# Optimization experiments

Measured on AMD Instinct MI355X. Metric: run time of the kernel, lower is better.

The kernel has to match this reference:

```python
import jax, jax.numpy as jnp
import numpy as np

N_NODES = 50000
N_EDGES = 800000
F_IN = 64
F_OUT = 64
SELF_LOOP_W = 2.0  # GCNConv improved=True


def setup_inputs() -> dict:
    key = jax.random.key(0)
    k1, k2, k3 = jax.random.split(key, 3)
    x = jax.random.normal(k1, (N_NODES, F_IN), dtype=jnp.float32)
    edge_index = jax.random.randint(k2, (2, N_EDGES), 0, N_NODES, dtype=jnp.int64)
    W = jax.random.normal(k3, (F_IN, F_OUT), dtype=jnp.float32) / np.sqrt(F_IN)
    b = jnp.zeros((F_OUT,), dtype=jnp.float32)
    return {"x": x, "edge_index": edge_index, "W": W, "b": b}


def reference(x, edge_index, W, b):
    N = x.shape[0]
    E = edge_index.shape[1]
    src, dst = edge_index[0], edge_index[1]
    # add self loops with weight 2.0 (improved=True)
    loop = jnp.arange(N, dtype=src.dtype)
    src_f = jnp.concatenate([src, loop])
    dst_f = jnp.concatenate([dst, loop])
    w_edge = jnp.concatenate([jnp.ones((E,), x.dtype), jnp.full((N,), SELF_LOOP_W, x.dtype)])
    # symmetric normalization: deg over target nodes (PyG gcn_norm)
    deg = jax.ops.segment_sum(w_edge, dst_f, num_segments=N)
    dinv = jnp.where(deg > 0, deg ** -0.5, 0.0)
    norm = dinv[src_f] * w_edge * dinv[dst_f]  # [E+N]
    # dense transform, then gather-scale-scatter
    h = x @ W  # [N, F_OUT]
    agg = jax.ops.segment_sum(norm[:, None] * h[src_f], dst_f, num_segments=N)
    out = jax.nn.relu(agg + b)
    return jax.nn.log_softmax(out, axis=1)
```

## Files before the change

kernel.cpp:

```cpp
#include <hip/hip_runtime.h>
#include <hip/hip_fp16.h>

#define N_NODES 50000
#define N_EDGES 800000
#define F 64
#define NB ((N_NODES + 255) / 256)
#define NBUCK 98
#define BSHIFT 9
#define BCAP 12288
#define P1_BLOCKS ((N_EDGES + 1023) / 1024)
#define NPB 32


union H2U { __half2 h; unsigned u; };

__global__ void k_init(int* __restrict__ bcur) {
    int t = threadIdx.x;
    if (t < NBUCK) bcur[t] = t * BCAP;
}

__global__ __launch_bounds__(1024) void k_p1(const int* __restrict__ src,
                                             const int* __restrict__ dst,
                                             int* __restrict__ bcur,
                                             int* __restrict__ staging) {
    __shared__ int lcnt[NBUCK];
    __shared__ int lbase[NBUCK];
    int t = threadIdx.x;
    if (t < NBUCK) lcnt[t] = 0;
    __syncthreads();
    int e = blockIdx.x * 1024 + t;
    int s = 0, d = 0, bk = 0, rank = 0;
    bool valid = (e < N_EDGES);
    if (valid) {
        s = src[e]; d = dst[e];
        bk = d >> BSHIFT;
        rank = atomicAdd(&lcnt[bk], 1);
    }
    __syncthreads();
    if (t < NBUCK && lcnt[t]) lbase[t] = atomicAdd(&bcur[t], lcnt[t]);
    __syncthreads();
    if (valid)
        staging[lbase[bk] + rank] = ((d & 511) << 16) | s;
}

__global__ __launch_bounds__(1024) void k_p23(const int* __restrict__ staging,
                                              const int* __restrict__ bcur,
                                              int* __restrict__ offsets,
                                              int* __restrict__ counts,
                                              float* __restrict__ dinv,
                                              int* __restrict__ pack) {
    __shared__ int ncnt[512];
    __shared__ int lcur[512];
    int t = threadIdx.x;
    int b = blockIdx.x;
    int nb0 = b << BSHIFT;
    if (t < 512) ncnt[t] = 0;
    __syncthreads();
    int beg = b * BCAP, end = bcur[b];
    for (int i = beg + t; i < end; i += 1024)
        atomicAdd(&ncnt[staging[i] >> 16], 1);
    __syncthreads();
    int c = (t < 512) ? ncnt[t] : 0;
    for (int off = 1; off < 512; off <<= 1) {
        int u = (t < 512 && t >= off) ? ncnt[t - off] : 0;
        __syncthreads();
        if (t < 512) ncnt[t] += u;
        __syncthreads();
    }
    if (t < 512) {
        int goff = beg + (ncnt[t] - c);
        lcur[t] = goff;
        int node = nb0 + t;
        if (node < N_NODES) {
            offsets[node] = goff;
            counts[node]  = c;
            dinv[node]    = rsqrtf((float)c + 2.0f);
        }
    }
    __syncthreads();
    for (int i = beg + t; i < end; i += 1024) {
        int v = staging[i];
        int pos = atomicAdd(&lcur[v >> 16], 1);
        pack[pos] = v & 0xFFFF;
    }
}

__global__ __launch_bounds__(256) void k_convert(const float4* __restrict__ x4,
                                                 uint2* __restrict__ xh8) {
    int t = blockIdx.x * 256 + threadIdx.x;
    float4 v = x4[t];
    H2U a, b;
    a.h = __float22half2_rn(make_float2(v.x, v.y));
    b.h = __float22half2_rn(make_float2(v.z, v.w));
    uint2 o; o.x = a.u; o.y = b.u;
    xh8[t] = o;
}

__global__ __launch_bounds__(512) void k_agg(const float* __restrict__ x,
                                             const __half* __restrict__ xh,
                                             const float* __restrict__ dinv,
                                             const int* __restrict__ offsets,
                                             const int* __restrict__ counts,
                                             const int* __restrict__ pack,
                                             const float* __restrict__ W,
                                             const float* __restrict__ bias,
                                             float* __restrict__ out) {
    __shared__ unsigned sWu[F * F / 2];
    __shared__ float srow[NPB][F];
    int t = threadIdx.x;
    for (int i = t; i < F * F / 2; i += 512) {
        int p = i >> 6, c = i & 63;
        H2U u;
        u.h = __float22half2_rn(make_float2(W[(2 * p) * F + c], W[(2 * p + 1) * F + c]));
        sWu[i] = u.u;
    }
    __syncthreads();

    int wid = t >> 6, lane = t & 63;
    int qe = lane >> 4, qc = lane & 15;
    int nbase = blockIdx.x * NPB + wid * 4;
    const uint2* xh8 = reinterpret_cast<const uint2*>(xh);

    int  begs[4], degs[4], pls[4];
    float dns[4], nms[4];
#pragma unroll
    for (int i = 0; i < 4; ++i) {
        int n = nbase + i;
        if (n < N_NODES) {
            begs[i] = offsets[n]; degs[i] = counts[n]; dns[i] = dinv[n];
        } else { begs[i] = 0; degs[i] = 0; dns[i] = 0.f; }
    }
#pragma unroll
    for (int i = 0; i < 4; ++i) {
        int s = 0; float nm = 0.f;
        if (lane < degs[i]) {
            s = pack[begs[i] + lane];
            nm = dns[i] * dinv[s];
        }
        pls[i] = s; nms[i] = nm;
    }

#pragma unroll
    for (int i = 0; i < 4; i += 2) {
        float a00 = 0.f, a01 = 0.f, a02 = 0.f, a03 = 0.f;
        float a10 = 0.f, a11 = 0.f, a12 = 0.f, a13 = 0.f;
        int lim = min(max(degs[i], degs[i + 1]), 64);
        for (int r = 0; r < lim; r += 8) {
            int e0 = r + qe, e1 = r + 4 + qe;
            int   s00 = __shfl(pls[i], e0);     float m00 = __shfl(nms[i], e0);
            int   s01 = __shfl(pls[i], e1);     float m01 = __shfl(nms[i], e1);
            int   s10 = __shfl(pls[i + 1], e0); float m10 = __shfl(nms[i + 1], e0);
            int   s11 = __shfl(pls[i + 1], e1); float m11 = __shfl(nms[i + 1], e1);
            uint2 v00 = xh8[(size_t)s00 * 16 + qc];
            uint2 v01 = xh8[(size_t)s01 * 16 + qc];
            uint2 v10 = xh8[(size_t)s10 * 16 + qc];
            uint2 v11 = xh8[(size_t)s11 * 16 + qc];
            H2U u0, u1; float2 f;
            u0.u = v00.x; u1.u = v00.y;
            f = __half22float2(u0.h); a00 = fmaf(m00, f.x, a00); a01 = fmaf(m00, f.y, a01);
            f = __half22float2(u1.h); a02 = fmaf(m00, f.x, a02); a03 = fmaf(m00, f.y, a03);
            u0.u = v01.x; u1.u = v01.y;
            f = __half22float2(u0.h); a00 = fmaf(m01, f.x, a00); a01 = fmaf(m01, f.y, a01);
            f = __half22float2(u1.h); a02 = fmaf(m01, f.x, a02); a03 = fmaf(m01, f.y, a03);
            u0.u = v10.x; u1.u = v10.y;
            f = __half22float2(u0.h); a10 = fmaf(m10, f.x, a10); a11 = fmaf(m10, f.y, a11);
            f = __half22float2(u1.h); a12 = fmaf(m10, f.x, a12); a13 = fmaf(m10, f.y, a13);
            u0.u = v11.x; u1.u = v11.y;
            f = __half22float2(u0.h); a10 = fmaf(m11, f.x, a10); a11 = fmaf(m11, f.y, a11);
            f = __half22float2(u1.h); a12 = fmaf(m11, f.x, a12); a13 = fmaf(m11, f.y, a13);
        }
#pragma unroll
        for (int k = 0; k < 2; ++k) {
            int dend = begs[i + k] + degs[i + k];
            for (int base = begs[i + k] + 64; base < dend; base += 8) {
                int e0 = base + qe, e1 = base + 4 + qe;
                int s0 = 0, s1 = 0; float m0 = 0.f, m1 = 0.f;
                if (e0 < dend) { s0 = pack[e0]; m0 = dns[i + k] * dinv[s0]; }
                if (e1 < dend) { s1 = pack[e1]; m1 = dns[i + k] * dinv[s1]; }
                uint2 r0 = xh8[(size_t)s0 * 16 + qc];
                uint2 r1 = xh8[(size_t)s1 * 16 + qc];
                H2U u0, u1; float2 f;
                float* A = (k == 0) ? &a00 : &a10;
                u0.u = r0.x; u1.u = r0.y;
                f = __half22float2(u0.h); A[0] = fmaf(m0, f.x, A[0]); A[1] = fmaf(m0, f.y, A[1]);
                f = __half22float2(u1.h); A[2] = fmaf(m0, f.x, A[2]); A[3] = fmaf(m0, f.y, A[3]);
                u0.u = r1.x; u1.u = r1.y;
                f = __half22float2(u0.h); A[0] = fmaf(m1, f.x, A[0]); A[1] = fmaf(m1, f.y, A[1]);
                f = __half22float2(u1.h); A[2] = fmaf(m1, f.x, A[2]); A[3] = fmaf(m1, f.y, A[3]);
            }
        }
        a00 += __shfl_xor(a00, 16); a10 += __shfl_xor(a10, 16);
        a01 += __shfl_xor(a01, 16); a11 += __shfl_xor(a11, 16);
        a02 += __shfl_xor(a02, 16); a12 += __shfl_xor(a12, 16);
        a03 += __shfl_xor(a03, 16); a13 += __shfl_xor(a13, 16);
        a00 += __shfl_xor(a00, 32); a10 += __shfl_xor(a10, 32);
        a01 += __shfl_xor(a01, 32); a11 += __shfl_xor(a11, 32);
        a02 += __shfl_xor(a02, 32); a12 += __shfl_xor(a12, 32);
        a03 += __shfl_xor(a03, 32); a13 += __shfl_xor(a13, 32);
        if (qe == 0) {
            int n0 = nbase + i;
            if (n0 < N_NODES) {
                float c2 = 2.0f * dns[i] * dns[i];
                float4 xv = reinterpret_cast<const float4*>(x + (size_t)n0 * F)[qc];
                a00 = fmaf(c2, xv.x, a00); a01 = fmaf(c2, xv.y, a01);
                a02 = fmaf(c2, xv.z, a02); a03 = fmaf(c2, xv.w, a03);
                float4 w; w.x = a00; w.y = a01; w.z = a02; w.w = a03;
                *reinterpret_cast<float4*>(&srow[wid * 4 + i][qc * 4]) = w;
            }
            int n1 = nbase + i + 1;
            if (n1 < N_NODES) {
                float c2 = 2.0f * dns[i + 1] * dns[i + 1];
                float4 xv = reinterpret_cast<const float4*>(x + (size_t)n1 * F)[qc];
                a10 = fmaf(c2, xv.x, a10); a11 = fmaf(c2, xv.y, a11);
                a12 = fmaf(c2, xv.z, a12); a13 = fmaf(c2, xv.w, a13);
                float4 w; w.x = a10; w.y = a11; w.z = a12; w.w = a13;
                *reinterpret_cast<float4*>(&srow[wid * 4 + i + 1][qc * 4]) = w;
            }
        }
    }

    asm volatile("s_waitcnt lgkmcnt(0)" ::: "memory");

    float bl = bias[lane];
    float y0 = bl, y1 = bl, y2 = bl, y3 = bl;
#pragma unroll 4
    for (int j = 0; j < 16; ++j) {
        float4 r0 = *reinterpret_cast<const float4*>(&srow[wid * 4 + 0][j * 4]);
        float4 r1 = *reinterpret_cast<const float4*>(&srow[wid * 4 + 1][j * 4]);
        float4 r2 = *reinterpret_cast<const float4*>(&srow[wid * 4 + 2][j * 4]);
        float4 r3 = *reinterpret_cast<const float4*>(&srow[wid * 4 + 3][j * 4]);
        H2U ua, ub;
        ua.u = sWu[(2 * j) * F + lane];
        ub.u = sWu[(2 * j + 1) * F + lane];
        float2 wab = __half22float2(ua.h);
        float2 wcd = __half22float2(ub.h);
        y0 = fmaf(r0.x, wab.x, y0); y0 = fmaf(r0.y, wab.y, y0); y0 = fmaf(r0.z, wcd.x, y0); y0 = fmaf(r0.w, wcd.y, y0);
        y1 = fmaf(r1.x, wab.x, y1); y1 = fmaf(r1.y, wab.y, y1); y1 = fmaf(r1.z, wcd.x, y1); y1 = fmaf(r1.w, wcd.y, y1);
        y2 = fmaf(r2.x, wab.x, y2); y2 = fmaf(r2.y, wab.y, y2); y2 = fmaf(r2.z, wcd.x, y2); y2 = fmaf(r2.w, wcd.y, y2);
        y3 = fmaf(r3.x, wab.x, y3); y3 = fmaf(r3.y, wab.y, y3); y3 = fmaf(r3.z, wcd.x, y3); y3 = fmaf(r3.w, wcd.y, y3);
    }

    float ys[4] = { y0, y1, y2, y3 };
#pragma unroll
    for (int i = 0; i < 4; ++i) {
        float y = fmaxf(ys[i], 0.0f);
        float mx = y;
#pragma unroll
        for (int off = 32; off > 0; off >>= 1)
            mx = fmaxf(mx, __shfl_xor(mx, off));
        float ex = __expf(y - mx);
        float ss = ex;
#pragma unroll
        for (int off = 32; off > 0; off >>= 1)
            ss += __shfl_xor(ss, off);
        int n = nbase + i;
        if (n < N_NODES) out[n * F + lane] = y - mx - __logf(ss);
    }
}


__global__ void k_count_b(const int* __restrict__ dst, int* __restrict__ counts) {
    int e = blockIdx.x * blockDim.x + threadIdx.x;
    if (e < N_EDGES) atomicAdd(&counts[dst[e]], 1);
}
__global__ __launch_bounds__(256) void k_blocksum(const int* __restrict__ counts,
                                                  int* __restrict__ bs) {
    __shared__ int sh[256];
    int t = threadIdx.x;
    int g = blockIdx.x * 256 + t;
    int v = (g < N_NODES) ? counts[g] : 0;
    sh[t] = v;
    __syncthreads();
    for (int off = 128; off > 0; off >>= 1) {
        if (t < off) sh[t] += sh[t + off];
        __syncthreads();
    }
    if (t == 0) bs[blockIdx.x] = sh[0];
}
__global__ __launch_bounds__(256) void k_scanblocks(int* __restrict__ bs) {
    __shared__ int sh[256];
    int t = threadIdx.x;
    int v = (t < NB) ? bs[t] : 0;
    sh[t] = v;
    __syncthreads();
    for (int off = 1; off < 256; off <<= 1) {
        int u = (t >= off) ? sh[t - off] : 0;
        __syncthreads();
        sh[t] += u;
        __syncthreads();
    }
    if (t < NB) bs[t] = sh[t] - v;
}
__global__ __launch_bounds__(256) void k_offsets_b(int* __restrict__ counts,
                                                   const int* __restrict__ bs,
                                                   int* __restrict__ offsets,
                                                   float* __restrict__ dinv) {
    __shared__ int sh[256];
    int t = threadIdx.x;
    int g = blockIdx.x * 256 + t;
    int c = (g < N_NODES) ? counts[g] : 0;
    sh[t] = c;
    __syncthreads();
    for (int off = 1; off < 256; off <<= 1) {
        int u = (t >= off) ? sh[t - off] : 0;
        __syncthreads();
        sh[t] += u;
        __syncthreads();
    }
    int excl = sh[t] - c + bs[blockIdx.x];
    if (g < N_NODES) {
        offsets[g] = excl;
        counts[g]  = excl;
        dinv[g]    = rsqrtf((float)c + 2.0f);
    }
    if (g == 0) offsets[N_NODES] = N_EDGES;
}
__global__ void k_fill_b(const int* __restrict__ src, const int* __restrict__ dst,
                         int* __restrict__ cursor, int* __restrict__ sorted_src) {
    int e = blockIdx.x * blockDim.x + threadIdx.x;
    if (e < N_EDGES) {
        int pos = atomicAdd(&cursor[dst[e]], 1);
        sorted_src[pos] = src[e];
    }
}
__global__ __launch_bounds__(256) void k_agg_b(const float* __restrict__ x,
                                               const float* __restrict__ dinv,
                                               const int* __restrict__ offsets,
                                               const int* __restrict__ sorted_src,
                                               const float* __restrict__ W,
                                               const float* __restrict__ b,
                                               float* __restrict__ out) {
    __shared__ float sW[F * F];
    __shared__ float srow[4][F];
    int t = threadIdx.x;
    for (int i = t; i < F * F; i += 256) sW[i] = W[i];
    int wid = t >> 6, lane = t & 63;
    int n = blockIdx.x * 4 + wid;
    int qe = lane >> 4, qc = lane & 15;
    float dn = dinv[n];
    int beg = offsets[n], end = offsets[n + 1];
    float4 acc = make_float4(0.f, 0.f, 0.f, 0.f);
    for (int base = beg; base < end; base += 4) {
        int e = base + qe;
        int s = n; float nm = 0.f;
        if (e < end) { s = sorted_src[e]; nm = dn * dinv[s]; }
        float4 v = reinterpret_cast<const float4*>(x + (size_t)s * F)[qc];
        acc.x = fmaf(nm, v.x, acc.x); acc.y = fmaf(nm, v.y, acc.y);
        acc.z = fmaf(nm, v.z, acc.z); acc.w = fmaf(nm, v.w, acc.w);
    }
    acc.x += __shfl_xor(acc.x, 16); acc.y += __shfl_xor(acc.y, 16);
    acc.z += __shfl_xor(acc.z, 16); acc.w += __shfl_xor(acc.w, 16);
    acc.x += __shfl_xor(acc.x, 32); acc.y += __shfl_xor(acc.y, 32);
    acc.z += __shfl_xor(acc.z, 32); acc.w += __shfl_xor(acc.w, 32);
    float c2 = 2.0f * dn * dn;
    float4 xv = reinterpret_cast<const float4*>(x + (size_t)n * F)[qc];
    acc.x = fmaf(c2, xv.x, acc.x); acc.y = fmaf(c2, xv.y, acc.y);
    acc.z = fmaf(c2, xv.z, acc.z); acc.w = fmaf(c2, xv.w, acc.w);
    if (qe == 0) reinterpret_cast<float4*>(&srow[wid][0])[qc] = acc;
    __syncthreads();
    float y = b[lane];
#pragma unroll
    for (int k = 0; k < F; ++k) y = fmaf(srow[wid][k], sW[k * F + lane], y);
    y = fmaxf(y, 0.0f);
    float m = y;
#pragma unroll
    for (int off = 32; off > 0; off >>= 1) m = fmaxf(m, __shfl_xor(m, off));
    float ex = __expf(y - m);
    float ss = ex;
#pragma unroll
    for (int off = 32; off > 0; off >>= 1) ss += __shfl_xor(ss, off);
    out[n * F + lane] = y - m - __logf(ss);
}


__global__ void k_init_deg_f(float* __restrict__ deg) {
    int i = blockIdx.x * blockDim.x + threadIdx.x;
    if (i < N_NODES) deg[i] = 2.0f;
}
__global__ void k_count_f(const int* __restrict__ dst, float* __restrict__ deg) {
    int e = blockIdx.x * blockDim.x + threadIdx.x;
    if (e < N_EDGES) atomicAdd(&deg[dst[e]], 1.0f);
}
__global__ void k_dinv_f(float* __restrict__ deg) {
    int i = blockIdx.x * blockDim.x + threadIdx.x;
    if (i < N_NODES) deg[i] = rsqrtf(deg[i]);
}
__global__ void k_selfinit_f(const float* __restrict__ x, const float* __restrict__ dinv,
                             float* __restrict__ agg) {
    int t = blockIdx.x * blockDim.x + threadIdx.x;
    if (t >= N_NODES * (F / 4)) return;
    int n = t >> 4;
    float d = dinv[n];
    float c = 2.0f * d * d;
    float4 v = reinterpret_cast<const float4*>(x)[t];
    float4 o; o.x = c*v.x; o.y = c*v.y; o.z = c*v.z; o.w = c*v.w;
    reinterpret_cast<float4*>(agg)[t] = o;
}
__global__ __launch_bounds__(256) void k_scatter_f(const int* __restrict__ src,
                                                   const int* __restrict__ dst,
                                                   const float* __restrict__ x,
                                                   const float* __restrict__ dinv,
                                                   float* __restrict__ agg) {
    int wave = (blockIdx.x * blockDim.x + threadIdx.x) >> 6;
    int lane = threadIdx.x & 63;
    if (wave >= N_EDGES) return;
    int s = src[wave], d = dst[wave];
    atomicAdd(&agg[d * F + lane], dinv[s] * dinv[d] * x[s * F + lane]);
}
__global__ __launch_bounds__(256) void k_final_f(const float* __restrict__ W,
                                                 const float* __restrict__ b,
                                                 float* __restrict__ out) {
    __shared__ float sW[F * F];
    __shared__ float srow[4][F];
    int t = threadIdx.x;
    for (int i = t; i < F * F; i += 256) sW[i] = W[i];
    int wid = t >> 6, lane = t & 63;
    int n = blockIdx.x * 4 + wid;
    float rv = out[n * F + lane];
    srow[wid][lane] = rv;
    __syncthreads();
    float y = b[lane];
#pragma unroll
    for (int k = 0; k < F; ++k) y = fmaf(srow[wid][k], sW[k * F + lane], y);
    y = fmaxf(y, 0.0f);
    float m = y;
#pragma unroll
    for (int off = 32; off > 0; off >>= 1) m = fmaxf(m, __shfl_xor(m, off));
    float ex = __expf(y - m);
    float ss = ex;
#pragma unroll
    for (int off = 32; off > 0; off >>= 1) ss += __shfl_xor(ss, off);
    out[n * F + lane] = y - m - __logf(ss);
}


extern "C" void kernel_launch(void* const* d_in, const int* in_sizes, int n_in,
                              void* d_out, int out_size, void* d_ws, size_t ws_size,
                              hipStream_t stream) {
    const float* x    = (const float*)d_in[0];
    const int*   eidx = (const int*)d_in[1];
    const float* W    = (const float*)d_in[2];
    const float* b    = (const float*)d_in[3];
    const int* src = eidx;
    const int* dst = eidx + N_EDGES;
    float* out = (float*)d_out;

    const size_t NEED_A4 = 11818112;
    const size_t NEED_B  = 3801040;

    if (ws_size >= NEED_A4) {
        char* ws = (char*)d_ws;
        int*    offsets = (int*)(ws);
        int*    counts  = (int*)(ws + 200064);
        float*  dinv    = (float*)(ws + 400128);
        int*    bcur    = (int*)(ws + 600192);
        int*    pack    = (int*)(ws + 601216);
        int*    staging = (int*)(ws + 5418112);
        __half* xh      = (__half*)(ws + 5418112);

        k_init<<<1, 128, 0, stream>>>(bcur);
        k_p1<<<P1_BLOCKS, 1024, 0, stream>>>(src, dst, bcur, staging);
        k_p23<<<NBUCK, 1024, 0, stream>>>(staging, bcur, offsets, counts, dinv, pack);
        k_convert<<<N_NODES * (F / 4) / 256, 256, 0, stream>>>((const float4*)x, (uint2*)xh);
        k_agg<<<(N_NODES + NPB - 1) / NPB, 512, 0, stream>>>(
            x, xh, dinv, offsets, counts, pack, W, b, out);
    } else if (ws_size >= NEED_B) {
        char* ws = (char*)d_ws;
        int*   counts     = (int*)(ws);
        int*   offsets    = (int*)(ws + 200000);
        float* dinv       = (float*)(ws + 400016);
        int*   bs         = (int*)(ws + 600016);
        int*   sorted_src = (int*)(ws + 601040);

        hipMemsetAsync(counts, 0, N_NODES * sizeof(int), stream);
        k_count_b<<<(N_EDGES + 255) / 256, 256, 0, stream>>>(dst, counts);
        k_blocksum<<<NB, 256, 0, stream>>>(counts, bs);
        k_scanblocks<<<1, 256, 0, stream>>>(bs);
        k_offsets_b<<<NB, 256, 0, stream>>>(counts, bs, offsets, dinv);
        k_fill_b<<<(N_EDGES + 255) / 256, 256, 0, stream>>>(src, dst, counts, sorted_src);
        k_agg_b<<<N_NODES / 4, 256, 0, stream>>>(x, dinv, offsets, sorted_src, W, b, out);
    } else {
        float* deg = (float*)d_ws;
        k_init_deg_f<<<(N_NODES + 255) / 256, 256, 0, stream>>>(deg);
        k_count_f<<<(N_EDGES + 255) / 256, 256, 0, stream>>>(dst, deg);
        k_dinv_f<<<(N_NODES + 255) / 256, 256, 0, stream>>>(deg);
        k_selfinit_f<<<(N_NODES * (F / 4) + 255) / 256, 256, 0, stream>>>(x, deg, out);
        k_scatter_f<<<(N_EDGES * 64 + 255) / 256, 256, 0, stream>>>(src, dst, x, deg, out);
        k_final_f<<<N_NODES / 4, 256, 0, stream>>>(W, b, out);
    }
}
```

Baseline: 86.70 us.

## Fuse fp16 conversion into bucketing pass and process four nodes per wave

Merges the x-to-fp16 conversion kernel into the edge bucketing kernel and replaces the bucket-counter init kernel with a memset. Staging now lives in the output buffer, so the staging region no longer aliases xh and the conversion can run early. The aggregation kernel loads node metadata with vector loads and interleaves gathers for all four nodes of a wave in one loop to raise memory-level parallelism. The cost is higher register pressure in the aggregation loop.

```diff
diff --git a/kernel.cpp b/kernel.cpp
--- a/kernel.cpp
+++ b/kernel.cpp
@@ -14,25 +14,30 @@
 
 union H2U { __half2 h; unsigned u; };
 
-__global__ void k_init(int* __restrict__ bcur) {
-    int t = threadIdx.x;
-    if (t < NBUCK) bcur[t] = t * BCAP;
-}
-
-__global__ __launch_bounds__(1024) void k_p1(const int* __restrict__ src,
-                                             const int* __restrict__ dst,
-                                             int* __restrict__ bcur,
-                                             int* __restrict__ staging) {
+__global__ __launch_bounds__(1024) void k_p1c(const int* __restrict__ src,
+                                              const int* __restrict__ dst,
+                                              int* __restrict__ bcur,
+                                              int* __restrict__ staging,
+                                              const float4* __restrict__ x4,
+                                              uint2* __restrict__ xh8) {
     __shared__ int lcnt[NBUCK];
     __shared__ int lbase[NBUCK];
     int t = threadIdx.x;
+    int g = blockIdx.x * 1024 + t;
     if (t < NBUCK) lcnt[t] = 0;
-    __syncthreads();
-    int e = blockIdx.x * 1024 + t;
+    if (g < N_NODES * (F / 4)) {
+        float4 v = x4[g];
+        H2U a, b;
+        a.h = __float22half2_rn(make_float2(v.x, v.y));
+        b.h = __float22half2_rn(make_float2(v.z, v.w));
+        uint2 o; o.x = a.u; o.y = b.u;
+        xh8[g] = o;
+    }
+    __syncthreads();
     int s = 0, d = 0, bk = 0, rank = 0;
-    bool valid = (e < N_EDGES);
+    bool valid = (g < N_EDGES);
     if (valid) {
-        s = src[e]; d = dst[e];
+        s = src[g]; d = dst[g];
         bk = d >> BSHIFT;
         rank = atomicAdd(&lcnt[bk], 1);
     }
@@ -40,7 +45,7 @@
     if (t < NBUCK && lcnt[t]) lbase[t] = atomicAdd(&bcur[t], lcnt[t]);
     __syncthreads();
     if (valid)
-        staging[lbase[bk] + rank] = ((d & 511) << 16) | s;
+        staging[bk * BCAP + lbase[bk] + rank] = ((d & 511) << 16) | s;
 }
 
 __global__ __launch_bounds__(1024) void k_p23(const int* __restrict__ staging,
@@ -56,7 +61,7 @@
     int nb0 = b << BSHIFT;
     if (t < 512) ncnt[t] = 0;
     __syncthreads();
-    int beg = b * BCAP, end = bcur[b];
+    int beg = b * BCAP, end = beg + bcur[b];
     for (int i = beg + t; i < end; i += 1024)
         atomicAdd(&ncnt[staging[i] >> 16], 1);
     __syncthreads();
@@ -83,17 +88,6 @@
         int pos = atomicAdd(&lcur[v >> 16], 1);
         pack[pos] = v & 0xFFFF;
     }
-}
-
-__global__ __launch_bounds__(256) void k_convert(const float4* __restrict__ x4,
-                                                 uint2* __restrict__ xh8) {
-    int t = blockIdx.x * 256 + threadIdx.x;
-    float4 v = x4[t];
-    H2U a, b;
-    a.h = __float22half2_rn(make_float2(v.x, v.y));
-    b.h = __float22half2_rn(make_float2(v.z, v.w));
-    uint2 o; o.x = a.u; o.y = b.u;
-    xh8[t] = o;
 }
 
 __global__ __launch_bounds__(512) void k_agg(const float* __restrict__ x,
@@ -121,15 +115,17 @@
     int nbase = blockIdx.x * NPB + wid * 4;
     const uint2* xh8 = reinterpret_cast<const uint2*>(xh);
 
-    int  begs[4], degs[4], pls[4];
-    float dns[4], nms[4];
-#pragma unroll
-    for (int i = 0; i < 4; ++i) {
-        int n = nbase + i;
-        if (n < N_NODES) {
-            begs[i] = offsets[n]; degs[i] = counts[n]; dns[i] = dinv[n];
-        } else { begs[i] = 0; degs[i] = 0; dns[i] = 0.f; }
-    }
+    int4   off4 = *reinterpret_cast<const int4*>(offsets + nbase);
+    int4   cnt4 = *reinterpret_cast<const int4*>(counts + nbase);
+    float4 dv4  = *reinterpret_cast<const float4*>(dinv + nbase);
+    int   begs[4] = { off4.x, off4.y, off4.z, off4.w };
+    int   degs[4] = { cnt4.x, cnt4.y, cnt4.z, cnt4.w };
+    float dns[4]  = { dv4.x, dv4.y, dv4.z, dv4.w };
+#pragma unroll
+    for (int i = 0; i < 4; ++i)
+        if (nbase + i >= N_NODES) { degs[i] = 0; dns[i] = 0.f; begs[i] = 0; }
+
+    int pls[4]; float nms[4];
 #pragma unroll
     for (int i = 0; i < 4; ++i) {
         int s = 0; float nm = 0.f;
@@ -140,81 +136,80 @@
         pls[i] = s; nms[i] = nm;
     }
 
-#pragma unroll
-    for (int i = 0; i < 4; i += 2) {
-        float a00 = 0.f, a01 = 0.f, a02 = 0.f, a03 = 0.f;
-        float a10 = 0.f, a11 = 0.f, a12 = 0.f, a13 = 0.f;
-        int lim = min(max(degs[i], degs[i + 1]), 64);
-        for (int r = 0; r < lim; r += 8) {
-            int e0 = r + qe, e1 = r + 4 + qe;
-            int   s00 = __shfl(pls[i], e0);     float m00 = __shfl(nms[i], e0);
-            int   s01 = __shfl(pls[i], e1);     float m01 = __shfl(nms[i], e1);
-            int   s10 = __shfl(pls[i + 1], e0); float m10 = __shfl(nms[i + 1], e0);
-            int   s11 = __shfl(pls[i + 1], e1); float m11 = __shfl(nms[i + 1], e1);
-            uint2 v00 = xh8[(size_t)s00 * 16 + qc];
-            uint2 v01 = xh8[(size_t)s01 * 16 + qc];
-            uint2 v10 = xh8[(size_t)s10 * 16 + qc];
-            uint2 v11 = xh8[(size_t)s11 * 16 + qc];
+    float acc[4][4];
+#pragma unroll
+    for (int i = 0; i < 4; ++i)
+#pragma unroll
+        for (int j = 0; j < 4; ++j) acc[i][j] = 0.f;
+
+    int lim = max(max(degs[0], degs[1]), max(degs[2], degs[3]));
+    lim = min(lim, 64);
+    for (int r = 0; r < lim; r += 8) {
+        int e0 = r + qe, e1 = r + 4 + qe;
+        uint2 v[4][2]; float m[4][2];
+#pragma unroll
+        for (int i = 0; i < 4; ++i) {
+            int s0 = __shfl(pls[i], e0); m[i][0] = __shfl(nms[i], e0);
+            int s1 = __shfl(pls[i], e1); m[i][1] = __shfl(nms[i], e1);
+            v[i][0] = xh8[(size_t)s0 * 16 + qc];
+            v[i][1] = xh8[(size_t)s1 * 16 + qc];
+        }
+#pragma unroll
+        for (int i = 0; i < 4; ++i)
+#pragma unroll
+            for (int j = 0; j < 2; ++j) {
+                H2U u0, u1;
+                u0.u = v[i][j].x; u1.u = v[i][j].y;
+                float2 f0 = __half22float2(u0.h);
+                float2 f1 = __half22float2(u1.h);
+                float mm = m[i][j];
+                acc[i][0] = fmaf(mm, f0.x, acc[i][0]);
+                acc[i][1] = fmaf(mm, f0.y, acc[i][1]);
+                acc[i][2] = fmaf(mm, f1.x, acc[i][2]);
+                acc[i][3] = fmaf(mm, f1.y, acc[i][3]);
+            }
+    }
+#pragma unroll
+    for (int i = 0; i < 4; ++i) {
+        int dend = begs[i] + degs[i];
+        for (int base = begs[i] + 64; base < dend; base += 8) {
+            int e0 = base + qe, e1 = base + 4 + qe;
+            int s0 = 0, s1 = 0; float m0 = 0.f, m1 = 0.f;
+            if (e0 < dend) { s0 = pack[e0]; m0 = dns[i] * dinv[s0]; }
+            if (e1 < dend) { s1 = pack[e1]; m1 = dns[i] * dinv[s1]; }
+            uint2 r0 = xh8[(size_t)s0 * 16 + qc];
+            uint2 r1 = xh8[(size_t)s1 * 16 + qc];
             H2U u0, u1; float2 f;
-            u0.u = v00.x; u1.u = v00.y;
-            f = __half22float2(u0.h); a00 = fmaf(m00, f.x, a00); a01 = fmaf(m00, f.y, a01);
-            f = __half22float2(u1.h); a02 = fmaf(m00, f.x, a02); a03 = fmaf(m00, f.y, a03);
-            u0.u = v01.x; u1.u = v01.y;
-            f = __half22float2(u0.h); a00 = fmaf(m01, f.x, a00); a01 = fmaf(m01, f.y, a01);
-            f = __half22float2(u1.h); a02 = fmaf(m01, f.x, a02); a03 = fmaf(m01, f.y, a03);
-            u0.u = v10.x; u1.u = v10.y;
-            f = __half22float2(u0.h); a10 = fmaf(m10, f.x, a10); a11 = fmaf(m10, f.y, a11);
-            f = __half22float2(u1.h); a12 = fmaf(m10, f.x, a12); a13 = fmaf(m10, f.y, a13);
-            u0.u = v11.x; u1.u = v11.y;
-            f = __half22float2(u0.h); a10 = fmaf(m11, f.x, a10); a11 = fmaf(m11, f.y, a11);
-            f = __half22float2(u1.h); a12 = fmaf(m11, f.x, a12); a13 = fmaf(m11, f.y, a13);
-        }
-#pragma unroll
-        for (int k = 0; k < 2; ++k) {
-            int dend = begs[i + k] + degs[i + k];
-            for (int base = begs[i + k] + 64; base < dend; base += 8) {
-                int e0 = base + qe, e1 = base + 4 + qe;
-                int s0 = 0, s1 = 0; float m0 = 0.f, m1 = 0.f;
-                if (e0 < dend) { s0 = pack[e0]; m0 = dns[i + k] * dinv[s0]; }
-                if (e1 < dend) { s1 = pack[e1]; m1 = dns[i + k] * dinv[s1]; }
-                uint2 r0 = xh8[(size_t)s0 * 16 + qc];
-                uint2 r1 = xh8[(size_t)s1 * 16 + qc];
-                H2U u0, u1; float2 f;
-                float* A = (k == 0) ? &a00 : &a10;
-                u0.u = r0.x; u1.u = r0.y;
-                f = __half22float2(u0.h); A[0] = fmaf(m0, f.x, A[0]); A[1] = fmaf(m0, f.y, A[1]);
-                f = __half22float2(u1.h); A[2] = fmaf(m0, f.x, A[2]); A[3] = fmaf(m0, f.y, A[3]);
-                u0.u = r1.x; u1.u = r1.y;
-                f = __half22float2(u0.h); A[0] = fmaf(m1, f.x, A[0]); A[1] = fmaf(m1, f.y, A[1]);
-                f = __half22float2(u1.h); A[2] = fmaf(m1, f.x, A[2]); A[3] = fmaf(m1, f.y, A[3]);
-            }
-        }
-        a00 += __shfl_xor(a00, 16); a10 += __shfl_xor(a10, 16);
-        a01 += __shfl_xor(a01, 16); a11 += __shfl_xor(a11, 16);
-        a02 += __shfl_xor(a02, 16); a12 += __shfl_xor(a12, 16);
-        a03 += __shfl_xor(a03, 16); a13 += __shfl_xor(a13, 16);
-        a00 += __shfl_xor(a00, 32); a10 += __shfl_xor(a10, 32);
-        a01 += __shfl_xor(a01, 32); a11 += __shfl_xor(a11, 32);
-        a02 += __shfl_xor(a02, 32); a12 += __shfl_xor(a12, 32);
-        a03 += __shfl_xor(a03, 32); a13 += __shfl_xor(a13, 32);
-        if (qe == 0) {
-            int n0 = nbase + i;
-            if (n0 < N_NODES) {
+            u0.u = r0.x; u1.u = r0.y;
+            f = __half22float2(u0.h); acc[i][0] = fmaf(m0, f.x, acc[i][0]); acc[i][1] = fmaf(m0, f.y, acc[i][1]);
+            f = __half22float2(u1.h); acc[i][2] = fmaf(m0, f.x, acc[i][2]); acc[i][3] = fmaf(m0, f.y, acc[i][3]);
+            u0.u = r1.x; u1.u = r1.y;
+            f = __half22float2(u0.h); acc[i][0] = fmaf(m1, f.x, acc[i][0]); acc[i][1] = fmaf(m1, f.y, acc[i][1]);
+            f = __half22float2(u1.h); acc[i][2] = fmaf(m1, f.x, acc[i][2]); acc[i][3] = fmaf(m1, f.y, acc[i][3]);
+        }
+    }
+
+#pragma unroll
+    for (int i = 0; i < 4; ++i)
+#pragma unroll
+        for (int j = 0; j < 4; ++j) {
+            acc[i][j] += __shfl_xor(acc[i][j], 16);
+            acc[i][j] += __shfl_xor(acc[i][j], 32);
+        }
+
+    if (qe == 0) {
+#pragma unroll
+        for (int i = 0; i < 4; ++i) {
+            int n = nbase + i;
+            if (n < N_NODES) {
                 float c2 = 2.0f * dns[i] * dns[i];
-                float4 xv = reinterpret_cast<const float4*>(x + (size_t)n0 * F)[qc];
-                a00 = fmaf(c2, xv.x, a00); a01 = fmaf(c2, xv.y, a01);
-                a02 = fmaf(c2, xv.z, a02); a03 = fmaf(c2, xv.w, a03);
-                float4 w; w.x = a00; w.y = a01; w.z = a02; w.w = a03;
+                float4 xv = reinterpret_cast<const float4*>(x + (size_t)n * F)[qc];
+                float4 w;
+                w.x = fmaf(c2, xv.x, acc[i][0]);
+                w.y = fmaf(c2, xv.y, acc[i][1]);
+                w.z = fmaf(c2, xv.z, acc[i][2]);
+                w.w = fmaf(c2, xv.w, acc[i][3]);
                 *reinterpret_cast<float4*>(&srow[wid * 4 + i][qc * 4]) = w;
-            }
-            int n1 = nbase + i + 1;
-            if (n1 < N_NODES) {
-                float c2 = 2.0f * dns[i + 1] * dns[i + 1];
-                float4 xv = reinterpret_cast<const float4*>(x + (size_t)n1 * F)[qc];
-                a10 = fmaf(c2, xv.x, a10); a11 = fmaf(c2, xv.y, a11);
-                a12 = fmaf(c2, xv.z, a12); a13 = fmaf(c2, xv.w, a13);
-                float4 w; w.x = a10; w.y = a11; w.z = a12; w.w = a13;
-                *reinterpret_cast<float4*>(&srow[wid * 4 + i + 1][qc * 4]) = w;
             }
         }
     }
@@ -445,23 +440,23 @@
     const int* dst = eidx + N_EDGES;
     float* out = (float*)d_out;
 
-    const size_t NEED_A4 = 11818112;
+    const size_t NEED_A5 = 11818112;
     const size_t NEED_B  = 3801040;
 
-    if (ws_size >= NEED_A4) {
+    if (ws_size >= NEED_A5) {
         char* ws = (char*)d_ws;
         int*    offsets = (int*)(ws);
         int*    counts  = (int*)(ws + 200064);
         float*  dinv    = (float*)(ws + 400128);
         int*    bcur    = (int*)(ws + 600192);
         int*    pack    = (int*)(ws + 601216);
-        int*    staging = (int*)(ws + 5418112);
         __half* xh      = (__half*)(ws + 5418112);
-
-        k_init<<<1, 128, 0, stream>>>(bcur);
-        k_p1<<<P1_BLOCKS, 1024, 0, stream>>>(src, dst, bcur, staging);
+        int*    staging = (int*)d_out;
+
+        hipMemsetAsync(bcur, 0, NBUCK * sizeof(int), stream);
+        k_p1c<<<P1_BLOCKS, 1024, 0, stream>>>(src, dst, bcur, staging,
+                                              (const float4*)x, (uint2*)xh);
         k_p23<<<NBUCK, 1024, 0, stream>>>(staging, bcur, offsets, counts, dinv, pack);
-        k_convert<<<N_NODES * (F / 4) / 256, 256, 0, stream>>>((const float4*)x, (uint2*)xh);
         k_agg<<<(N_NODES + NPB - 1) / NPB, 512, 0, stream>>>(
             x, xh, dinv, offsets, counts, pack, W, b, out);
     } else if (ws_size >= NEED_B) {
```

Result: slower. 89.97 us (+3.8%).

## Fuse fp16 conversion into edge bucketing and stage edges in output buffer

Applied to the files above, without the earlier changes.

Merges the fp32-to-fp16 conversion of x into the edge bucketing kernel, which removes one kernel launch. The bucket cursor is now relative and zeroed with a memset instead of an init kernel. The staging area moves into the output buffer, so it no longer aliases xh. The aggregation kernel reads the self-loop term from the fp16 copy rather than fp32 x, and loads offsets, counts and dinv as vectors. This lowers launch overhead and memory traffic, at the cost of slightly lower self-loop precision and reliance on out not being read before k_agg writes it.

```diff
diff --git a/kernel.cpp b/kernel.cpp
--- a/kernel.cpp
+++ b/kernel.cpp
@@ -14,25 +14,30 @@
 
 union H2U { __half2 h; unsigned u; };
 
-__global__ void k_init(int* __restrict__ bcur) {
-    int t = threadIdx.x;
-    if (t < NBUCK) bcur[t] = t * BCAP;
-}
-
-__global__ __launch_bounds__(1024) void k_p1(const int* __restrict__ src,
-                                             const int* __restrict__ dst,
-                                             int* __restrict__ bcur,
-                                             int* __restrict__ staging) {
+__global__ __launch_bounds__(1024) void k_p1c(const int* __restrict__ src,
+                                              const int* __restrict__ dst,
+                                              int* __restrict__ bcur,
+                                              int* __restrict__ staging,
+                                              const float4* __restrict__ x4,
+                                              uint2* __restrict__ xh8) {
     __shared__ int lcnt[NBUCK];
     __shared__ int lbase[NBUCK];
     int t = threadIdx.x;
+    int g = blockIdx.x * 1024 + t;
     if (t < NBUCK) lcnt[t] = 0;
-    __syncthreads();
-    int e = blockIdx.x * 1024 + t;
+    if (g < N_NODES * (F / 4)) {
+        float4 v = x4[g];
+        H2U a, b;
+        a.h = __float22half2_rn(make_float2(v.x, v.y));
+        b.h = __float22half2_rn(make_float2(v.z, v.w));
+        uint2 o; o.x = a.u; o.y = b.u;
+        xh8[g] = o;
+    }
+    __syncthreads();
     int s = 0, d = 0, bk = 0, rank = 0;
-    bool valid = (e < N_EDGES);
+    bool valid = (g < N_EDGES);
     if (valid) {
-        s = src[e]; d = dst[e];
+        s = src[g]; d = dst[g];
         bk = d >> BSHIFT;
         rank = atomicAdd(&lcnt[bk], 1);
     }
@@ -40,7 +45,7 @@
     if (t < NBUCK && lcnt[t]) lbase[t] = atomicAdd(&bcur[t], lcnt[t]);
     __syncthreads();
     if (valid)
-        staging[lbase[bk] + rank] = ((d & 511) << 16) | s;
+        staging[bk * BCAP + lbase[bk] + rank] = ((d & 511) << 16) | s;
 }
 
 __global__ __launch_bounds__(1024) void k_p23(const int* __restrict__ staging,
@@ -56,7 +61,7 @@
     int nb0 = b << BSHIFT;
     if (t < 512) ncnt[t] = 0;
     __syncthreads();
-    int beg = b * BCAP, end = bcur[b];
+    int beg = b * BCAP, end = beg + bcur[b];
     for (int i = beg + t; i < end; i += 1024)
         atomicAdd(&ncnt[staging[i] >> 16], 1);
     __syncthreads();
@@ -85,19 +90,7 @@
     }
 }
 
-__global__ __launch_bounds__(256) void k_convert(const float4* __restrict__ x4,
-                                                 uint2* __restrict__ xh8) {
-    int t = blockIdx.x * 256 + threadIdx.x;
-    float4 v = x4[t];
-    H2U a, b;
-    a.h = __float22half2_rn(make_float2(v.x, v.y));
-    b.h = __float22half2_rn(make_float2(v.z, v.w));
-    uint2 o; o.x = a.u; o.y = b.u;
-    xh8[t] = o;
-}
-
-__global__ __launch_bounds__(512) void k_agg(const float* __restrict__ x,
-                                             const __half* __restrict__ xh,
+__global__ __launch_bounds__(512) void k_agg(const __half* __restrict__ xh,
                                              const float* __restrict__ dinv,
                                              const int* __restrict__ offsets,
                                              const int* __restrict__ counts,
@@ -121,15 +114,17 @@
     int nbase = blockIdx.x * NPB + wid * 4;
     const uint2* xh8 = reinterpret_cast<const uint2*>(xh);
 
-    int  begs[4], degs[4], pls[4];
-    float dns[4], nms[4];
-#pragma unroll
-    for (int i = 0; i < 4; ++i) {
-        int n = nbase + i;
-        if (n < N_NODES) {
-            begs[i] = offsets[n]; degs[i] = counts[n]; dns[i] = dinv[n];
-        } else { begs[i] = 0; degs[i] = 0; dns[i] = 0.f; }
-    }
+    int4   off4 = *reinterpret_cast<const int4*>(offsets + nbase);
+    int4   cnt4 = *reinterpret_cast<const int4*>(counts + nbase);
+    float4 dv4  = *reinterpret_cast<const float4*>(dinv + nbase);
+    int   begs[4] = { off4.x, off4.y, off4.z, off4.w };
+    int   degs[4] = { cnt4.x, cnt4.y, cnt4.z, cnt4.w };
+    float dns[4]  = { dv4.x, dv4.y, dv4.z, dv4.w };
+#pragma unroll
+    for (int i = 0; i < 4; ++i)
+        if (nbase + i >= N_NODES) { degs[i] = 0; dns[i] = 0.f; begs[i] = 0; }
+
+    int pls[4]; float nms[4];
 #pragma unroll
     for (int i = 0; i < 4; ++i) {
         int s = 0; float nm = 0.f;
@@ -201,19 +196,25 @@
             int n0 = nbase + i;
             if (n0 < N_NODES) {
                 float c2 = 2.0f * dns[i] * dns[i];
-                float4 xv = reinterpret_cast<const float4*>(x + (size_t)n0 * F)[qc];
-                a00 = fmaf(c2, xv.x, a00); a01 = fmaf(c2, xv.y, a01);
-                a02 = fmaf(c2, xv.z, a02); a03 = fmaf(c2, xv.w, a03);
-                float4 w; w.x = a00; w.y = a01; w.z = a02; w.w = a03;
+                uint2 hv = xh8[(size_t)n0 * 16 + qc];
+                H2U u0, u1; u0.u = hv.x; u1.u = hv.y;
+                float2 f0 = __half22float2(u0.h);
+                float2 f1 = __half22float2(u1.h);
+                float4 w;
+                w.x = fmaf(c2, f0.x, a00); w.y = fmaf(c2, f0.y, a01);
+                w.z = fmaf(c2, f1.x, a02); w.w = fmaf(c2, f1.y, a03);
                 *reinterpret_cast<float4*>(&srow[wid * 4 + i][qc * 4]) = w;
             }
             int n1 = nbase + i + 1;
             if (n1 < N_NODES) {
                 float c2 = 2.0f * dns[i + 1] * dns[i + 1];
-                float4 xv = reinterpret_cast<const float4*>(x + (size_t)n1 * F)[qc];
-                a10 = fmaf(c2, xv.x, a10); a11 = fmaf(c2, xv.y, a11);
-                a12 = fmaf(c2, xv.z, a12); a13 = fmaf(c2, xv.w, a13);
-                float4 w; w.x = a10; w.y = a11; w.z = a12; w.w = a13;
+                uint2 hv = xh8[(size_t)n1 * 16 + qc];
+                H2U u0, u1; u0.u = hv.x; u1.u = hv.y;
+                float2 f0 = __half22float2(u0.h);
+                float2 f1 = __half22float2(u1.h);
+                float4 w;
+                w.x = fmaf(c2, f0.x, a10); w.y = fmaf(c2, f0.y, a11);
+                w.z = fmaf(c2, f1.x, a12); w.w = fmaf(c2, f1.y, a13);
                 *reinterpret_cast<float4*>(&srow[wid * 4 + i + 1][qc * 4]) = w;
             }
         }
@@ -445,25 +446,25 @@
     const int* dst = eidx + N_EDGES;
     float* out = (float*)d_out;
 
-    const size_t NEED_A4 = 11818112;
+    const size_t NEED_A6 = 11818112;
     const size_t NEED_B  = 3801040;
 
-    if (ws_size >= NEED_A4) {
+    if (ws_size >= NEED_A6) {
         char* ws = (char*)d_ws;
         int*    offsets = (int*)(ws);
         int*    counts  = (int*)(ws + 200064);
         float*  dinv    = (float*)(ws + 400128);
         int*    bcur    = (int*)(ws + 600192);
         int*    pack    = (int*)(ws + 601216);
-        int*    staging = (int*)(ws + 5418112);
         __half* xh      = (__half*)(ws + 5418112);
-
-        k_init<<<1, 128, 0, stream>>>(bcur);
-        k_p1<<<P1_BLOCKS, 1024, 0, stream>>>(src, dst, bcur, staging);
+        int*    staging = (int*)d_out;
+
+        hipMemsetAsync(bcur, 0, NBUCK * sizeof(int), stream);
+        k_p1c<<<P1_BLOCKS, 1024, 0, stream>>>(src, dst, bcur, staging,
+                                              (const float4*)x, (uint2*)xh);
         k_p23<<<NBUCK, 1024, 0, stream>>>(staging, bcur, offsets, counts, dinv, pack);
-        k_convert<<<N_NODES * (F / 4) / 256, 256, 0, stream>>>((const float4*)x, (uint2*)xh);
         k_agg<<<(N_NODES + NPB - 1) / NPB, 512, 0, stream>>>(
-            x, xh, dinv, offsets, counts, pack, W, b, out);
+            xh, dinv, offsets, counts, pack, W, b, out);
     } else if (ws_size >= NEED_B) {
         char* ws = (char*)d_ws;
         int*   counts     = (int*)(ws);
```

Measured after the change: 83.03 us. 4.2% less time.
